# Kernel optimization log

Hardware: AMD Instinct MI355X
Metric: run time of the kernel (lower is better)

Reference implementation:

```python
import jax, jax.numpy as jnp
import numpy as np

B, N, M, MENU = 1024, 16, 16, 256


def setup_inputs() -> dict:
    key = jax.random.key(0)
    k0, k1, k2, k3, k4 = jax.random.split(key, 5)
    input_bids = jax.random.uniform(k0, (B, N, M), dtype=jnp.float32)
    input_values = jax.random.uniform(k1, (B, N, M), dtype=jnp.float32)
    allocs = jax.random.uniform(k2, (B, MENU, N, M), dtype=jnp.float32)
    # w must be strictly positive (1/w appears in payments); shift away from 0
    w = jax.random.uniform(k3, (B, N), dtype=jnp.float32) + 0.5
    b = jax.random.normal(k4, (B, MENU), dtype=jnp.float32) * 0.1
    return {
        "input_bids": input_bids,
        "input_values": input_values,
        "allocs": allocs,
        "w": w,
        "b": b,
        "softmax_temp": 500,
    }


def reference(input_bids, input_values, allocs, w, b, softmax_temp):
    Bx, n, m = input_bids.shape
    temp = jnp.asarray(softmax_temp, dtype=input_bids.dtype)
    value_bid = input_values - input_bids                      # [B,n,m]
    # append the all-zero "null" allocation option (menu size K = MENU+1)
    allocs_p = jnp.concatenate(
        [allocs, jnp.zeros((Bx, 1, n, m), allocs.dtype)], axis=1)  # [B,K,n,m]
    b_p = jnp.concatenate([b, jnp.zeros((Bx, 1), b.dtype)], axis=1)  # [B,K]

    util = jnp.einsum('bknm,bnm->bkn', allocs_p, value_bid)    # [B,K,n]
    per_agent_welfare = w[:, None, :] * util                   # [B,K,n]
    total_welfare = per_agent_welfare.sum(-1)                  # [B,K]

    alloc_choice = jax.nn.softmax((total_welfare + b_p) * temp, axis=-1)  # [B,K]
    item_allocation = jnp.einsum('bk,bknm->bnm', alloc_choice, allocs_p)  # [B,n,m]
    chosen_paw = jnp.einsum('bk,bkn->bn', alloc_choice, per_agent_welfare)  # [B,n]
    chosen_sum = chosen_paw.sum(-1)                            # [B]
    alloc_b = (alloc_choice * b_p).sum(-1)                     # [B]

    # counterfactual: remove agent i -> welfare drops by per_agent_welfare[:,:,i]
    total_removed = total_welfare[None, :, :] - jnp.moveaxis(per_agent_welfare, 2, 0)  # [n,B,K]
    removed_choice = jax.nn.softmax((total_removed + b_p[None]) * temp, axis=-1)       # [n,B,K]
    removed_chosen_sum = jnp.einsum('ibk,ibk->ib', removed_choice, total_removed)      # [n,B]
    removed_b = jnp.einsum('ibk,bk->ib', removed_choice, b_p)                          # [n,B]

    payments = ((chosen_sum + alloc_b)[None, :]
                - (removed_chosen_sum + removed_b)) / w.T       # [n,B]
    bid_rev = (item_allocation * input_bids).sum(-1).T          # [n,B]
    payments = payments + bid_rev
    utility = (input_values * item_allocation).sum(-1).T - payments  # [n,B]

    return (alloc_choice, item_allocation, utility, payments, allocs_p, bid_rev)
```

## Files before the change

### kernel.cpp

```cpp
#include <hip/hip_runtime.h>
#include <math.h>

#define BX   1024
#define NA   16
#define NM   16
#define MENU 256
#define KK   257

typedef float v4f __attribute__((ext_vector_type(4)));

__global__ __launch_bounds__(256) void auction_kernel(
    const float* __restrict__ bids,
    const float* __restrict__ values,
    const float* __restrict__ allocs,
    const float* __restrict__ w,
    const float* __restrict__ bvec,
    const int*   __restrict__ tptr,
    float* __restrict__ out)
{
    const int b   = blockIdx.x;
    const int tid = threadIdx.x;

    __shared__ __align__(16) float vb[256];
    __shared__ float wl[16];
    __shared__ float paw[KK][17];
    __shared__ float tw_s[KK];
    __shared__ float bp_s[KK];
    __shared__ float ch_s[KK];
    __shared__ float red[8];

    int iv = *tptr;
    float temp = (iv > 0 && iv < (1 << 24)) ? (float)iv : __int_as_float(iv);

    float* out_choice  = out;
    float* out_item    = out + (size_t)BX * KK;
    float* out_util    = out_item + (size_t)BX * 256;
    float* out_pay     = out_util + (size_t)NA * BX;
    float* out_allocsp = out_pay  + (size_t)NA * BX;
    float* out_bidrev  = out_allocsp + (size_t)BX * KK * 256;

    vb[tid]   = values[(size_t)b * 256 + tid] - bids[(size_t)b * 256 + tid];
    bp_s[tid] = bvec[(size_t)b * 256 + tid];
    #pragma unroll
    for (int n2 = 0; n2 < 16; ++n2) paw[tid][n2] = 0.0f;
    if (tid < 16) { wl[tid] = w[b * 16 + tid]; paw[MENU][tid] = 0.0f; }
    if (tid == 0) { bp_s[MENU] = 0.0f; tw_s[MENU] = 0.0f; }
    __syncthreads();

    {
        const v4f* arow = (const v4f*)(allocs + (size_t)b * MENU * 256);
        v4f*       orow = (v4f*)(out_allocsp + (size_t)b * KK * 256);
        const int ksub = tid >> 6;
        const int l    = tid & 63;
        const v4f vb4  = ((const v4f*)vb)[l];
        const int n    = l >> 2;
        const float wn = wl[n];
        #pragma unroll 8
        for (int kb = 0; kb < 64; ++kb) {
            int k = kb * 4 + ksub;
            v4f a = arow[k * 64 + l];
            __builtin_nontemporal_store(a, orow + k * 64 + l);
            float d = a.x * vb4.x + a.y * vb4.y + a.z * vb4.z + a.w * vb4.w;
            atomicAdd(&paw[k][n], d * wn);
        }
        if (tid < 64) {
            v4f z = (v4f){0.f, 0.f, 0.f, 0.f};
            __builtin_nontemporal_store(z, orow + MENU * 64 + tid);
        }
    }
    __syncthreads();

    float tw = 0.0f;
    #pragma unroll
    for (int n = 0; n < 16; ++n) tw += paw[tid][n];
    tw_s[tid] = tw;
    const float logit = (tw + bp_s[tid]) * temp;

    const int wid = tid >> 6;
    float mx = logit;
    #pragma unroll
    for (int off = 32; off; off >>= 1) mx = fmaxf(mx, __shfl_xor(mx, off));
    if ((tid & 63) == 0) red[wid] = mx;
    __syncthreads();
    mx = fmaxf(fmaxf(red[0], red[1]), fmaxf(red[2], red[3]));
    mx = fmaxf(mx, 0.0f);

    float e = __expf(logit - mx);
    float s = e;
    #pragma unroll
    for (int off = 32; off; off >>= 1) s += __shfl_xor(s, off);
    if ((tid & 63) == 0) red[4 + wid] = s;
    __syncthreads();
    s = red[4] + red[5] + red[6] + red[7] + __expf(0.0f - mx);
    const float inv = 1.0f / s;

    const float c = e * inv;
    ch_s[tid] = c;
    out_choice[(size_t)b * KK + tid] = c;
    if (tid == 0) {
        float cn = __expf(0.0f - mx) * inv;
        ch_s[MENU] = cn;
        out_choice[(size_t)b * KK + MENU] = cn;
    }

    float q = c * (tw + bp_s[tid]);
    #pragma unroll
    for (int off = 32; off; off >>= 1) q += __shfl_xor(q, off);
    __syncthreads();
    if ((tid & 63) == 0) red[wid] = q;
    __syncthreads();
    const float cs_ab = red[0] + red[1] + red[2] + red[3];

    const int ai = tid >> 4;
    const int aj = tid & 15;
    float m1 = -1e30f;
    for (int k = aj; k < KK; k += 16) {
        float tr = tw_s[k] - paw[k][ai];
        m1 = fmaxf(m1, (tr + bp_s[k]) * temp);
    }
    #pragma unroll
    for (int off = 8; off; off >>= 1) m1 = fmaxf(m1, __shfl_xor(m1, off));
    float ss = 0.f, srs = 0.f, srb = 0.f;
    for (int k = aj; k < KK; k += 16) {
        float tr = tw_s[k] - paw[k][ai];
        float bp = bp_s[k];
        float eo = __expf((tr + bp) * temp - m1);
        ss  += eo;
        srs += eo * tr;
        srb += eo * bp;
    }
    #pragma unroll
    for (int off = 8; off; off >>= 1) {
        ss  += __shfl_xor(ss, off);
        srs += __shfl_xor(srs, off);
        srb += __shfl_xor(srb, off);
    }
    float paypre = 0.0f;
    if (aj == 0) paypre = (cs_ab - (srs + srb) / ss) / wl[ai];

    float ia = 0.0f;
    const float* ab = allocs + (size_t)b * MENU * 256 + tid;
    for (int k = 0; k < MENU; ++k) {
        float cc = ch_s[k];
        if (cc > 1e-9f) ia += cc * ab[(size_t)k * 256];
    }
    out_item[(size_t)b * 256 + tid] = ia;

    float pb = ia * bids[(size_t)b * 256 + tid];
    float pv = ia * values[(size_t)b * 256 + tid];
    #pragma unroll
    for (int off = 1; off <= 8; off <<= 1) {
        pb += __shfl_xor(pb, off);
        pv += __shfl_xor(pv, off);
    }
    if (aj == 0) {
        float pay = paypre + pb;
        out_bidrev[(size_t)ai * BX + b] = pb;
        out_pay[(size_t)ai * BX + b]    = pay;
        out_util[(size_t)ai * BX + b]   = pv - pay;
    }
}

extern "C" void kernel_launch(void* const* d_in, const int* in_sizes, int n_in,
                              void* d_out, int out_size, void* d_ws, size_t ws_size,
                              hipStream_t stream) {
    (void)in_sizes; (void)n_in; (void)d_ws; (void)ws_size; (void)out_size;
    const float* bids   = (const float*)d_in[0];
    const float* values = (const float*)d_in[1];
    const float* allocs = (const float*)d_in[2];
    const float* w      = (const float*)d_in[3];
    const float* bvec   = (const float*)d_in[4];
    const int*   tptr   = (const int*)d_in[5];
    float* out = (float*)d_out;

    auction_kernel<<<BX, 256, 0, stream>>>(bids, values, allocs, w, bvec, tptr, out);
}
```

Baseline: 137.4 us.

## Split auction into streaming copy kernel and per-batch tail kernel

Moves the large allocs copy and per-agent welfare dot products into a separate kernel with four blocks per batch row, which writes partial welfare to workspace. A second kernel loads those values and runs the softmax, counterfactual and payment logic. The LDS atomics are replaced by quad shuffle reductions, and the nontemporal stores become plain stores. This adds a second launch and a workspace round trip, and it only takes effect when the workspace is large enough, otherwise a fallback single kernel runs.

After: 140.9 us. 2.5% more time.

```diff
diff --git a/kernel.cpp b/kernel.cpp
--- a/kernel.cpp
+++ b/kernel.cpp
@@ -9,19 +9,61 @@
 
 typedef float v4f __attribute__((ext_vector_type(4)));
 
-__global__ __launch_bounds__(256) void auction_kernel(
+#define OFF_CHOICE  0
+#define OFF_ITEM    ((size_t)BX * KK)
+#define OFF_UTIL    (OFF_ITEM + (size_t)BX * 256)
+#define OFF_PAY     (OFF_UTIL + (size_t)NA * BX)
+#define OFF_ALLOCSP (OFF_PAY  + (size_t)NA * BX)
+#define OFF_BIDREV  (OFF_ALLOCSP + (size_t)BX * KK * 256)
+
+__global__ __launch_bounds__(256) void stream_kernel(
+    const float* __restrict__ bids,
+    const float* __restrict__ values,
+    const float* __restrict__ allocs,
+    const float* __restrict__ w,
+    float* __restrict__ out,
+    float* __restrict__ paw_ws)
+{
+    const int bid  = blockIdx.x;
+    const int b    = bid >> 2;
+    const int q    = bid & 3;
+    const int tid  = threadIdx.x;
+    const int wave = tid >> 6;
+    const int l    = tid & 63;
+
+    const v4f vb4 = ((const v4f*)(values + (size_t)b * 256))[l]
+                  - ((const v4f*)(bids   + (size_t)b * 256))[l];
+    const float wn = w[b * 16 + (l >> 2)];
+
+    const v4f* arow = (const v4f*)(allocs + (size_t)b * MENU * 256) + (size_t)q * 4096;
+    v4f*       orow = (v4f*)(out + OFF_ALLOCSP + (size_t)b * KK * 256) + (size_t)q * 4096;
+    float*     pw   = paw_ws + (size_t)b * 4096 + q * 1024;
+
+    #pragma unroll 8
+    for (int kb = 0; kb < 16; ++kb) {
+        const int k = kb * 4 + wave;
+        v4f a = arow[k * 64 + l];
+        orow[k * 64 + l] = a;
+        float d = a.x * vb4.x + a.y * vb4.y + a.z * vb4.z + a.w * vb4.w;
+        d += __shfl_xor(d, 1);
+        d += __shfl_xor(d, 2);
+        if ((l & 3) == 0) pw[k * 16 + (l >> 2)] = wn * d;
+    }
+}
+
+__global__ __launch_bounds__(256) void tail_kernel(
     const float* __restrict__ bids,
     const float* __restrict__ values,
     const float* __restrict__ allocs,
     const float* __restrict__ w,
     const float* __restrict__ bvec,
     const int*   __restrict__ tptr,
+    const float* __restrict__ paw_ws,
     float* __restrict__ out)
 {
     const int b   = blockIdx.x;
     const int tid = threadIdx.x;
 
-    __shared__ __align__(16) float vb[256];
     __shared__ float wl[16];
     __shared__ float paw[KK][17];
     __shared__ float tw_s[KK];
@@ -32,43 +74,32 @@
     int iv = *tptr;
     float temp = (iv > 0 && iv < (1 << 24)) ? (float)iv : __int_as_float(iv);
 
-    float* out_choice  = out;
-    float* out_item    = out + (size_t)BX * KK;
-    float* out_util    = out_item + (size_t)BX * 256;
-    float* out_pay     = out_util + (size_t)NA * BX;
-    float* out_allocsp = out_pay  + (size_t)NA * BX;
-    float* out_bidrev  = out_allocsp + (size_t)BX * KK * 256;
-
-    vb[tid]   = values[(size_t)b * 256 + tid] - bids[(size_t)b * 256 + tid];
+    float* out_choice  = out + OFF_CHOICE;
+    float* out_item    = out + OFF_ITEM;
+    float* out_util    = out + OFF_UTIL;
+    float* out_pay     = out + OFF_PAY;
+    float* out_allocsp = out + OFF_ALLOCSP;
+    float* out_bidrev  = out + OFF_BIDREV;
+
+    if (tid < 64) {
+        v4f z = (v4f){0.f, 0.f, 0.f, 0.f};
+        ((v4f*)(out_allocsp + (size_t)b * KK * 256 + (size_t)MENU * 256))[tid] = z;
+    }
+
+    {
+        const v4f* pws = (const v4f*)(paw_ws + (size_t)b * 4096);
+        #pragma unroll
+        for (int j = 0; j < 4; ++j) {
+            v4f t = pws[tid * 4 + j];
+            paw[tid][j * 4 + 0] = t.x;
+            paw[tid][j * 4 + 1] = t.y;
+            paw[tid][j * 4 + 2] = t.z;
+            paw[tid][j * 4 + 3] = t.w;
+        }
+    }
     bp_s[tid] = bvec[(size_t)b * 256 + tid];
-    #pragma unroll
-    for (int n2 = 0; n2 < 16; ++n2) paw[tid][n2] = 0.0f;
     if (tid < 16) { wl[tid] = w[b * 16 + tid]; paw[MENU][tid] = 0.0f; }
     if (tid == 0) { bp_s[MENU] = 0.0f; tw_s[MENU] = 0.0f; }
-    __syncthreads();
-
-    {
-        const v4f* arow = (const v4f*)(allocs + (size_t)b * MENU * 256);
-        v4f*       orow = (v4f*)(out_allocsp + (size_t)b * KK * 256);
-        const int ksub = tid >> 6;
-        const int l    = tid & 63;
-        const v4f vb4  = ((const v4f*)vb)[l];
-        const int n    = l >> 2;
-        const float wn = wl[n];
-        #pragma unroll 8
-        for (int kb = 0; kb < 64; ++kb) {
-            int k = kb * 4 + ksub;
-            v4f a = arow[k * 64 + l];
-            __builtin_nontemporal_store(a, orow + k * 64 + l);
-            float d = a.x * vb4.x + a.y * vb4.y + a.z * vb4.z + a.w * vb4.w;
-            atomicAdd(&paw[k][n], d * wn);
-        }
-        if (tid < 64) {
-            v4f z = (v4f){0.f, 0.f, 0.f, 0.f};
-            __builtin_nontemporal_store(z, orow + MENU * 64 + tid);
-        }
-    }
-    __syncthreads();
 
     float tw = 0.0f;
     #pragma unroll
@@ -103,11 +134,11 @@
         out_choice[(size_t)b * KK + MENU] = cn;
     }
 
-    float q = c * (tw + bp_s[tid]);
-    #pragma unroll
-    for (int off = 32; off; off >>= 1) q += __shfl_xor(q, off);
-    __syncthreads();
-    if ((tid & 63) == 0) red[wid] = q;
+    float qv = c * (tw + bp_s[tid]);
+    #pragma unroll
+    for (int off = 32; off; off >>= 1) qv += __shfl_xor(qv, off);
+    __syncthreads();
+    if ((tid & 63) == 0) red[wid] = qv;
     __syncthreads();
     const float cs_ab = red[0] + red[1] + red[2] + red[3];
 
@@ -161,10 +192,155 @@
     }
 }
 
+__global__ __launch_bounds__(256) void auction_kernel(
+    const float* __restrict__ bids, const float* __restrict__ values,
+    const float* __restrict__ allocs, const float* __restrict__ w,
+    const float* __restrict__ bvec, const int* __restrict__ tptr,
+    float* __restrict__ out)
+{
+    const int b   = blockIdx.x;
+    const int tid = threadIdx.x;
+
+    __shared__ __align__(16) float vb[256];
+    __shared__ float wl[16];
+    __shared__ float paw[KK][17];
+    __shared__ float tw_s[KK];
+    __shared__ float bp_s[KK];
+    __shared__ float ch_s[KK];
+    __shared__ float red[8];
+
+    int iv = *tptr;
+    float temp = (iv > 0 && iv < (1 << 24)) ? (float)iv : __int_as_float(iv);
+
+    float* out_choice  = out + OFF_CHOICE;
+    float* out_item    = out + OFF_ITEM;
+    float* out_util    = out + OFF_UTIL;
+    float* out_pay     = out + OFF_PAY;
+    float* out_allocsp = out + OFF_ALLOCSP;
+    float* out_bidrev  = out + OFF_BIDREV;
+
+    vb[tid]   = values[(size_t)b * 256 + tid] - bids[(size_t)b * 256 + tid];
+    bp_s[tid] = bvec[(size_t)b * 256 + tid];
+    if (tid < 16) { wl[tid] = w[b * 16 + tid]; paw[MENU][tid] = 0.0f; }
+    if (tid == 0) { bp_s[MENU] = 0.0f; tw_s[MENU] = 0.0f; }
+    __syncthreads();
+
+    {
+        const v4f* arow = (const v4f*)(allocs + (size_t)b * MENU * 256);
+        v4f*       orow = (v4f*)(out_allocsp + (size_t)b * KK * 256);
+        const int ksub = tid >> 6;
+        const int l    = tid & 63;
+        const v4f vb4  = ((const v4f*)vb)[l];
+        const float wn = wl[l >> 2];
+        #pragma unroll 8
+        for (int kb = 0; kb < 64; ++kb) {
+            int k = kb * 4 + ksub;
+            v4f a = arow[k * 64 + l];
+            orow[k * 64 + l] = a;
+            float d = a.x * vb4.x + a.y * vb4.y + a.z * vb4.z + a.w * vb4.w;
+            d += __shfl_xor(d, 1);
+            d += __shfl_xor(d, 2);
+            if ((l & 3) == 0) paw[k][l >> 2] = wn * d;
+        }
+        if (tid < 64) orow[MENU * 64 + tid] = (v4f){0.f, 0.f, 0.f, 0.f};
+    }
+    __syncthreads();
+
+    float tw = 0.0f;
+    #pragma unroll
+    for (int n = 0; n < 16; ++n) tw += paw[tid][n];
+    tw_s[tid] = tw;
+    const float logit = (tw + bp_s[tid]) * temp;
+
+    const int wid = tid >> 6;
+    float mx = logit;
+    #pragma unroll
+    for (int off = 32; off; off >>= 1) mx = fmaxf(mx, __shfl_xor(mx, off));
+    if ((tid & 63) == 0) red[wid] = mx;
+    __syncthreads();
+    mx = fmaxf(fmaxf(red[0], red[1]), fmaxf(red[2], red[3]));
+    mx = fmaxf(mx, 0.0f);
+
+    float e = __expf(logit - mx);
+    float s = e;
+    #pragma unroll
+    for (int off = 32; off; off >>= 1) s += __shfl_xor(s, off);
+    if ((tid & 63) == 0) red[4 + wid] = s;
+    __syncthreads();
+    s = red[4] + red[5] + red[6] + red[7] + __expf(0.0f - mx);
+    const float inv = 1.0f / s;
+
+    const float c = e * inv;
+    ch_s[tid] = c;
+    out_choice[(size_t)b * KK + tid] = c;
+    if (tid == 0) {
+        float cn = __expf(0.0f - mx) * inv;
+        ch_s[MENU] = cn;
+        out_choice[(size_t)b * KK + MENU] = cn;
+    }
+
+    float qv = c * (tw + bp_s[tid]);
+    #pragma unroll
+    for (int off = 32; off; off >>= 1) qv += __shfl_xor(qv, off);
+    __syncthreads();
+    if ((tid & 63) == 0) red[wid] = qv;
+    __syncthreads();
+    const float cs_ab = red[0] + red[1] + red[2] + red[3];
+
+    const int ai = tid >> 4;
+    const int aj = tid & 15;
+    float m1 = -1e30f;
+    for (int k = aj; k < KK; k += 16) {
+        float tr = tw_s[k] - paw[k][ai];
+        m1 = fmaxf(m1, (tr + bp_s[k]) * temp);
+    }
+    #pragma unroll
+    for (int off = 8; off; off >>= 1) m1 = fmaxf(m1, __shfl_xor(m1, off));
+    float ss = 0.f, srs = 0.f, srb = 0.f;
+    for (int k = aj; k < KK; k += 16) {
+        float tr = tw_s[k] - paw[k][ai];
+        float bp = bp_s[k];
+        float eo = __expf((tr + bp) * temp - m1);
+        ss  += eo;
+        srs += eo * tr;
+        srb += eo * bp;
+    }
+    #pragma unroll
+    for (int off = 8; off; off >>= 1) {
+        ss  += __shfl_xor(ss, off);
+        srs += __shfl_xor(srs, off);
+        srb += __shfl_xor(srb, off);
+    }
+    float paypre = 0.0f;
+    if (aj == 0) paypre = (cs_ab - (srs + srb) / ss) / wl[ai];
+
+    float ia = 0.0f;
+    const float* ab = allocs + (size_t)b * MENU * 256 + tid;
+    for (int k = 0; k < MENU; ++k) {
+        float cc = ch_s[k];
+        if (cc > 1e-9f) ia += cc * ab[(size_t)k * 256];
+    }
+    out_item[(size_t)b * 256 + tid] = ia;
+
+    float pb = ia * bids[(size_t)b * 256 + tid];
+    float pv = ia * values[(size_t)b * 256 + tid];
+    #pragma unroll
+    for (int off = 1; off <= 8; off <<= 1) {
+        pb += __shfl_xor(pb, off);
+        pv += __shfl_xor(pv, off);
+    }
+    if (aj == 0) {
+        float pay = paypre + pb;
+        out_bidrev[(size_t)ai * BX + b] = pb;
+        out_pay[(size_t)ai * BX + b]    = pay;
+        out_util[(size_t)ai * BX + b]   = pv - pay;
+    }
+}
+
 extern "C" void kernel_launch(void* const* d_in, const int* in_sizes, int n_in,
                               void* d_out, int out_size, void* d_ws, size_t ws_size,
                               hipStream_t stream) {
-    (void)in_sizes; (void)n_in; (void)d_ws; (void)ws_size; (void)out_size;
+    (void)in_sizes; (void)n_in; (void)out_size;
     const float* bids   = (const float*)d_in[0];
     const float* values = (const float*)d_in[1];
     const float* allocs = (const float*)d_in[2];
@@ -173,5 +349,12 @@
     const int*   tptr   = (const int*)d_in[5];
     float* out = (float*)d_out;
 
-    auction_kernel<<<BX, 256, 0, stream>>>(bids, values, allocs, w, bvec, tptr, out);
+    const size_t paw_bytes = (size_t)BX * 4096 * sizeof(float);
+    if (ws_size >= paw_bytes) {
+        float* paw_ws = (float*)d_ws;
+        stream_kernel<<<BX * 4, 256, 0, stream>>>(bids, values, allocs, w, out, paw_ws);
+        tail_kernel<<<BX, 256, 0, stream>>>(bids, values, allocs, w, bvec, tptr, paw_ws, out);
+    } else {
+        auction_kernel<<<BX, 256, 0, stream>>>(bids, values, allocs, w, bvec, tptr, out);
+    }
 }
```
